# Performance work log

Hardware: AMD Instinct MI355X
Metric: run time of the kernel (lower is better)

Reference implementation:

```python
import jax, jax.numpy as jnp
import numpy as np

# ---- constants from __init__ ----
DT = 1.0
NX, NY = 192, 192
SRC_X, SRC_Y = 40, 96
PX = jnp.array([160, 160, 160])
PY = jnp.array([48, 96, 144])
PML_N, PML_P, PML_MAX = 20, 4.0, 3.0
C0, C1 = 1.0, 0.9
H = DT * 2.01 / 1.0  # grid spacing


def make_b():
    """PML damping profile b(x,y), [NX, NY]."""
    v = (PML_MAX * np.linspace(0.0, 1.0, PML_N + 1) ** PML_P).astype(np.float32)
    bx = np.zeros((NX, NY), np.float32)
    bx[: PML_N + 1, :] = v[::-1, None]
    bx[NX - PML_N - 1 :, :] = v[:, None]
    by = np.zeros((NX, NY), np.float32)
    by[:, : PML_N + 1] = v[::-1][None, :]
    by[:, NY - PML_N - 1 :] = v[None, :]
    return jnp.asarray(np.sqrt(bx ** 2 + by ** 2))


def _conv3(img, kern):
    # img [B,1,H,W], kern [1,1,3,3], 'same' padding
    return jax.lax.conv_general_dilated(
        img, kern, (1, 1), ((1, 1), (1, 1)),
        dimension_numbers=("NCHW", "OIHW", "NCHW"))


def _proj(x, eta=0.5, beta=100.0):
    return (jnp.tanh(beta * eta) + jnp.tanh(beta * (x - eta))) / (
        jnp.tanh(beta * eta) + jnp.tanh(beta * (1.0 - eta)))


def setup_inputs() -> dict:
    key = jax.random.key(0)
    k1, k2 = jax.random.split(key)
    x = jax.random.normal(k1, (4, 256), dtype=jnp.float32)  # [batch, T]
    rho = jax.random.uniform(k2, (NX, NY), dtype=jnp.float32)
    # clip_pml_rho(): rho[b != 0] = 0 for binarized model (applied at init)
    rho = jnp.where(make_b() != 0, 0.0, rho)
    return {"x": x, "rho": rho}


def reference(x, rho):
    b = make_b()
    lpf_k = jnp.array([[[[0.0, 0.125, 0.0], [0.125, 0.5, 0.125], [0.0, 0.125, 0.0]]]], jnp.float32)
    lap_k = (H ** -2) * jnp.array([[[[0.0, 1.0, 0.0], [1.0, -4.0, 1.0], [0.0, 1.0, 0.0]]]], jnp.float32)
    A1 = 1.0 / (DT ** -2 + b * 0.5 / DT)
    A2 = 2.0 * DT ** -2
    A3 = DT ** -2 - b * 0.5 / DT

    # binarized wave-speed field c(rho): LPF then tanh projection
    lpf_rho = _conv3(rho[None, None], lpf_k)[0, 0]
    c = C0 + (C1 - C0) * _proj(lpf_rho)
    c2 = c * c

    B = x.shape[0]
    y0 = jnp.zeros((B, NX, NY), x.dtype)

    def step(carry, xi):
        y1, y2 = carry
        lap = _conv3(y1[:, None], lap_k)[:, 0]            # [B,NX,NY]
        y = A1 * (A2 * y1 - A3 * y2 + c2 * lap)
        y = y.at[:, SRC_X, SRC_Y].add(xi)                 # source injection
        return (y, y1), y[:, PX, PY]                      # emit probe values [B,P]

    _, probes = jax.lax.scan(step, (y0, y0), x.T)         # probes [T,B,P]

    # integrate_probe_points: sum |y|^2 over time, normalize per batch
    I = jnp.sum(probes ** 2, axis=0)                      # [B,P]
    return I / jnp.sum(I, axis=1, keepdims=True)
```

## Files before the change

### kernel.cpp

```cpp
#include <hip/hip_runtime.h>
#include <math.h>

#define NXY    192
#define CELLS  (NXY*NXY)
#define NBATCH 4
#define NSTEPS 256
#define TCH    16
#define NCHUNK (NSTEPS/TCH)
#define TPB    512
#define NW     8
#define RPL    5
#define OUTR   6
#define NBLKS  256

#define K3_OFF (16*CELLS)
#define Q_OFF  (K3_OFF + CELLS)
#define I_OFF  (Q_OFF + CELLS)

typedef float v2f __attribute__((ext_vector_type(2)));

__device__ __forceinline__ float dpp_up1(float v) {
    int r = __builtin_amdgcn_update_dpp(0, __builtin_bit_cast(int, v),
                                        0x138, 0xf, 0xf, true);
    return __builtin_bit_cast(float, r);
}
__device__ __forceinline__ float dpp_dn1(float v) {
    int r = __builtin_amdgcn_update_dpp(0, __builtin_bit_cast(int, v),
                                        0x130, 0xf, 0xf, true);
    return __builtin_bit_cast(float, r);
}

__device__ __forceinline__ float pml_prof(int i) {
    int t;
    if (i <= 20)            t = 20 - i;
    else if (i >= NXY - 21) t = i - (NXY - 21);
    else                    return 0.0f;
    float u  = (float)t * 0.05f;
    float u2 = u * u;
    return 3.0f * u2 * u2;
}

__global__ void setup_k(const float* __restrict__ rho, float* __restrict__ ws) {
    int idx    = blockIdx.x * blockDim.x + threadIdx.x;
    int stride = gridDim.x * blockDim.x;
    for (int k = idx; k < 8 * CELLS; k += stride) ws[k] = 0.0f;
    const float IH2 = (float)(1.0 / (2.01 * 2.01));
    for (int k = idx; k < CELLS; k += stride) {
        int i = k / NXY, j = k % NXY;
        float r0 = rho[k];
        float ru = (i > 0)       ? rho[k - NXY] : 0.0f;
        float rd = (i < NXY - 1) ? rho[k + NXY] : 0.0f;
        float rl = (j > 0)       ? rho[k - 1]   : 0.0f;
        float rr2 = (j < NXY - 1) ? rho[k + 1]  : 0.0f;
        float lpf = 0.5f * r0 + 0.125f * ((ru + rd) + (rl + rr2));
        float p   = 0.5f * (1.0f + tanhf(100.0f * (lpf - 0.5f)));
        float c   = 1.0f - 0.1f * p;
        float c2h = c * c * IH2;
        float bx = pml_prof(i), by = pml_prof(j);
        float bb = sqrtf(bx * bx + by * by);
        float a1 = 1.0f / (1.0f + 0.5f * bb);
        ws[K3_OFF + k] = a1 * c2h;
        ws[Q_OFF  + k] = 1.0f - 2.0f * a1;
    }
    if (idx < 12) ws[I_OFF + idx] = 0.0f;
}

__global__ __launch_bounds__(TPB, 1)
void chunk_k(const float* __restrict__ x, float* __restrict__ ws, int chunk) {
    int blk = blockIdx.x;
    int b  = blk / 64;
    int r_ = blk % 64;
    int bi = r_ >> 1, cj = r_ & 1;
    int I0 = OUTR * bi - 17;
    int J0 = 96 * cj - 16;
    int t  = threadIdx.x;
    int w  = t >> 6;
    int l  = t & 63;
    int row0 = I0 + RPL * w;
    int gj   = J0 + 2 * l;

    __shared__ v2f hb[2][2][NW + 2][64];
    for (int k = t; k < 2 * 2 * (NW + 2) * 64; k += TPB)
        ((v2f*)hb)[k] = (v2f){0.f, 0.f};

    float xv[TCH];
    int xbase = b * NSTEPS + chunk * TCH;
#pragma unroll
    for (int i = 0; i < TCH; i++) xv[i] = x[xbase + i];

    const float* kg = ws + K3_OFF;
    const float* qg = ws + Q_OFF;
    int pin = chunk & 1, pout = pin ^ 1;
    const float* curg  = ws + ((pin  * 2 + 0) * NBATCH + b) * CELLS;
    const float* prvg  = ws + ((pin  * 2 + 1) * NBATCH + b) * CELLS;
    float*       ncurg = ws + ((pout * 2 + 0) * NBATCH + b) * CELLS;
    float*       nprvg = ws + ((pout * 2 + 1) * NBATCH + b) * CELLS;

    v2f yc[RPL], yp[RPL], Qa[RPL], Ka[RPL];
    bool cok = (gj >= 0 && gj < NXY);
#pragma unroll
    for (int r = 0; r < RPL; r++) {
        int gi = row0 + r;
        bool ok = cok && gi >= 0 && gi < NXY;
        v2f kv = {0.f,0.f}, qv = {0.f,0.f}, cv = {0.f,0.f}, pv = {0.f,0.f};
        if (ok) {
            int idx = gi * NXY + gj;
            kv = *(const v2f*)(kg + idx);
            qv = *(const v2f*)(qg + idx);
            cv = *(const v2f*)(curg + idx);
            pv = *(const v2f*)(prvg + idx);
        }
        yc[r] = cv; yp[r] = pv; Ka[r] = kv; Qa[r] = qv;
    }

    int sr = 40 - I0, sc = 96 - J0;
    bool wave_src = (sr >= RPL * w) && (sr < RPL * w + RPL);
    int src_rl = sr - RPL * w;
    float srcm = (2 * l == sc) ? 1.f : 0.f;

    int pcl = 2 * l + J0;
    bool wave_prb = (bi == 26) && (w == 4);
    const int prb_rl = 1;
    bool is_prb = (cj == 0) ? (pcl == 48) : (pcl == 96 || pcl == 144);
    float prbm = is_prb ? 1.f : 0.f;
    float pacc = 0.f;

    v2f uph, dnh;

#define ROWC(CUR, PRV, rr_, UP, DN, XSV, YN) do {                              \
    v2f cv = CUR[rr_];                                                         \
    float lf0 = dpp_up1(cv.y);                                                 \
    float rt1 = dpp_dn1(cv.x);                                                 \
    v2f h = (v2f){lf0, rt1} + __builtin_shufflevector(cv, cv, 1, 0);           \
    v2f S = ((UP) + (DN)) + h;                                                 \
    YN = cv + Qa[rr_] * (PRV[rr_] - cv) + Ka[rr_] * (S - 4.0f * cv);           \
    if (wave_src && (rr_) == src_rl) YN.x += srcm * (XSV);                     \
    if (wave_prb && (rr_) == prb_rl) { float q = prbm * YN.x; pacc += q * YN.x; } \
} while (0)

#define STEP(CUR, PRV, PH, SIDX) do {                                          \
    v2f t0, t4;                                                                \
    ROWC(CUR, PRV, 0, uph,    CUR[1], xv[SIDX], t0);                           \
    ROWC(CUR, PRV, 4, CUR[3], dnh,    xv[SIDX], t4);                           \
    hb[PH][0][w + 1][l] = t0;                                                  \
    hb[PH][1][w + 1][l] = t4;                                                  \
    PRV[0] = t0; PRV[4] = t4;                                                  \
    _Pragma("unroll")                                                          \
    for (int r = 1; r <= 3; r++) {                                             \
        v2f y;                                                                 \
        ROWC(CUR, PRV, r, CUR[r - 1], CUR[r + 1], xv[SIDX], y);                \
        PRV[r] = y;                                                            \
    }                                                                          \
    __syncthreads();                                                           \
    uph = hb[PH][1][w][l];                                                     \
    dnh = hb[PH][0][w + 2][l];                                                 \
} while (0)

    hb[0][0][w + 1][l] = yc[0];
    hb[0][1][w + 1][l] = yc[4];
    __syncthreads();
    uph = hb[0][1][w][l];
    dnh = hb[0][0][w + 2][l];

#pragma unroll
    for (int s2 = 0; s2 < TCH / 2; s2++) {
        STEP(yc, yp, 1, 2 * s2);
        STEP(yp, yc, 0, 2 * s2 + 1);
    }
#undef STEP
#undef ROWC

#pragma unroll
    for (int r = 0; r < RPL; r++) {
        int gi = row0 + r;
        if (gi >= OUTR * bi && gi < OUTR * bi + OUTR && l >= 8 && l < 56) {
            int idx = gi * NXY + gj;
            *(v2f*)(ncurg + idx) = yc[r];
            *(v2f*)(nprvg + idx) = yp[r];
        }
    }
    if (wave_prb && is_prb)
        ws[I_OFF + b * 3 + (pcl / 48 - 1)] += pacc;
}

__global__ void final_k(const float* __restrict__ ws, float* __restrict__ out) {
    int t = threadIdx.x;
    if (t < 12) {
        const float* I = ws + I_OFF;
        int b = t / 3;
        float s = I[3 * b] + I[3 * b + 1] + I[3 * b + 2];
        out[t] = I[t] / s;
    }
}

extern "C" void kernel_launch(void* const* d_in, const int* in_sizes, int n_in,
                              void* d_out, int out_size, void* d_ws, size_t ws_size,
                              hipStream_t stream) {
    const float* x   = (const float*)d_in[0];
    const float* rho = (const float*)d_in[1];
    float* ws  = (float*)d_ws;
    float* out = (float*)d_out;

    setup_k<<<256, 256, 0, stream>>>(rho, ws);
    for (int c = 0; c < NCHUNK; c++)
        chunk_k<<<NBLKS, TPB, 0, stream>>>(x, ws, c);
    final_k<<<1, 64, 0, stream>>>(ws, out);
}
```

Before: 203.0 us.

## Fuse setup, chunked steps and finalize into one persistent cooperative kernel

Replaces the setup kernel, the 16 per-chunk launches and the final kernel with a single cooperative launch that loops over chunks, using grid.sync between chunks. Each block now computes its own K/Q coefficients from rho in registers, which drops the global coefficient arrays and the workspace zeroing. It also keeps x in shared memory and remaps block indices across XCDs. The intent is to remove per-launch overhead and redundant global traffic, in exchange for grid-wide barrier cost and a requirement that all 256 blocks be co-resident.

```diff
diff --git a/kernel.cpp b/kernel.cpp
--- a/kernel.cpp
+++ b/kernel.cpp
@@ -1,5 +1,8 @@
 #include <hip/hip_runtime.h>
+#include <hip/hip_cooperative_groups.h>
 #include <math.h>
+
+namespace cg = cooperative_groups;
 
 #define NXY    192
 #define CELLS  (NXY*NXY)
@@ -13,9 +16,7 @@
 #define OUTR   6
 #define NBLKS  256
 
-#define K3_OFF (16*CELLS)
-#define Q_OFF  (K3_OFF + CELLS)
-#define I_OFF  (Q_OFF + CELLS)
+#define I_OFF  (16*CELLS)
 
 typedef float v2f __attribute__((ext_vector_type(2)));
 
@@ -40,34 +41,12 @@
     return 3.0f * u2 * u2;
 }
 
-__global__ void setup_k(const float* __restrict__ rho, float* __restrict__ ws) {
-    int idx    = blockIdx.x * blockDim.x + threadIdx.x;
-    int stride = gridDim.x * blockDim.x;
-    for (int k = idx; k < 8 * CELLS; k += stride) ws[k] = 0.0f;
-    const float IH2 = (float)(1.0 / (2.01 * 2.01));
-    for (int k = idx; k < CELLS; k += stride) {
-        int i = k / NXY, j = k % NXY;
-        float r0 = rho[k];
-        float ru = (i > 0)       ? rho[k - NXY] : 0.0f;
-        float rd = (i < NXY - 1) ? rho[k + NXY] : 0.0f;
-        float rl = (j > 0)       ? rho[k - 1]   : 0.0f;
-        float rr2 = (j < NXY - 1) ? rho[k + 1]  : 0.0f;
-        float lpf = 0.5f * r0 + 0.125f * ((ru + rd) + (rl + rr2));
-        float p   = 0.5f * (1.0f + tanhf(100.0f * (lpf - 0.5f)));
-        float c   = 1.0f - 0.1f * p;
-        float c2h = c * c * IH2;
-        float bx = pml_prof(i), by = pml_prof(j);
-        float bb = sqrtf(bx * bx + by * by);
-        float a1 = 1.0f / (1.0f + 0.5f * bb);
-        ws[K3_OFF + k] = a1 * c2h;
-        ws[Q_OFF  + k] = 1.0f - 2.0f * a1;
-    }
-    if (idx < 12) ws[I_OFF + idx] = 0.0f;
-}
-
 __global__ __launch_bounds__(TPB, 1)
-void chunk_k(const float* __restrict__ x, float* __restrict__ ws, int chunk) {
-    int blk = blockIdx.x;
+void wave_k(const float* __restrict__ x, const float* __restrict__ rho,
+            float* __restrict__ ws, float* __restrict__ out) {
+    cg::grid_group grid = cg::this_grid();
+
+    int blk = ((blockIdx.x & 7) << 5) | (blockIdx.x >> 3);
     int b  = blk / 64;
     int r_ = blk % 64;
     int bi = r_ >> 1, cj = r_ & 1;
@@ -80,38 +59,60 @@
     int gj   = J0 + 2 * l;
 
     __shared__ v2f hb[2][2][NW + 2][64];
+    __shared__ float xs[NSTEPS];
     for (int k = t; k < 2 * 2 * (NW + 2) * 64; k += TPB)
         ((v2f*)hb)[k] = (v2f){0.f, 0.f};
-
-    float xv[TCH];
-    int xbase = b * NSTEPS + chunk * TCH;
-#pragma unroll
-    for (int i = 0; i < TCH; i++) xv[i] = x[xbase + i];
-
-    const float* kg = ws + K3_OFF;
-    const float* qg = ws + Q_OFF;
-    int pin = chunk & 1, pout = pin ^ 1;
-    const float* curg  = ws + ((pin  * 2 + 0) * NBATCH + b) * CELLS;
-    const float* prvg  = ws + ((pin  * 2 + 1) * NBATCH + b) * CELLS;
-    float*       ncurg = ws + ((pout * 2 + 0) * NBATCH + b) * CELLS;
-    float*       nprvg = ws + ((pout * 2 + 1) * NBATCH + b) * CELLS;
-
-    v2f yc[RPL], yp[RPL], Qa[RPL], Ka[RPL];
+    if (t < NSTEPS) xs[t] = x[b * NSTEPS + t];
+
     bool cok = (gj >= 0 && gj < NXY);
-#pragma unroll
-    for (int r = 0; r < RPL; r++) {
-        int gi = row0 + r;
-        bool ok = cok && gi >= 0 && gi < NXY;
-        v2f kv = {0.f,0.f}, qv = {0.f,0.f}, cv = {0.f,0.f}, pv = {0.f,0.f};
-        if (ok) {
-            int idx = gi * NXY + gj;
-            kv = *(const v2f*)(kg + idx);
-            qv = *(const v2f*)(qg + idx);
-            cv = *(const v2f*)(curg + idx);
-            pv = *(const v2f*)(prvg + idx);
-        }
-        yc[r] = cv; yp[r] = pv; Ka[r] = kv; Qa[r] = qv;
+
+    v2f Ka[RPL], Qa[RPL];
+    {
+        v2f rv[RPL + 2];
+#pragma unroll
+        for (int r = 0; r < RPL + 2; r++) {
+            int gi = row0 - 1 + r;
+            bool ok = cok && gi >= 0 && gi < NXY;
+            rv[r] = ok ? *(const v2f*)(rho + gi * NXY + gj) : (v2f){0.f, 0.f};
+        }
+        const float IH2 = (float)(1.0 / (2.01 * 2.01));
+#pragma unroll
+        for (int r = 0; r < RPL; r++) {
+            int gi = row0 + r;
+            v2f rc = rv[r + 1], ru = rv[r], rd = rv[r + 2];
+            float lf = dpp_up1(rc.y);
+            float rt = dpp_dn1(rc.x);
+            float bx = pml_prof(gi);
+            v2f K, Q;
+            {
+                float lpf = 0.5f * rc.x + 0.125f * ((ru.x + rd.x) + (lf + rc.y));
+                float p   = 0.5f * (1.0f + tanhf(100.0f * (lpf - 0.5f)));
+                float c   = 1.0f - 0.1f * p;
+                float by  = pml_prof(gj);
+                float bb  = sqrtf(bx * bx + by * by);
+                float a1  = 1.0f / (1.0f + 0.5f * bb);
+                K.x = a1 * (c * c * IH2);
+                Q.x = 1.0f - 2.0f * a1;
+            }
+            {
+                float lpf = 0.5f * rc.y + 0.125f * ((ru.y + rd.y) + (rc.x + rt));
+                float p   = 0.5f * (1.0f + tanhf(100.0f * (lpf - 0.5f)));
+                float c   = 1.0f - 0.1f * p;
+                float by  = pml_prof(gj + 1);
+                float bb  = sqrtf(bx * bx + by * by);
+                float a1  = 1.0f / (1.0f + 0.5f * bb);
+                K.y = a1 * (c * c * IH2);
+                Q.y = 1.0f - 2.0f * a1;
+            }
+            bool ok = cok && gi >= 0 && gi < NXY;
+            Ka[r] = ok ? K : (v2f){0.f, 0.f};
+            Qa[r] = ok ? Q : (v2f){0.f, 0.f};
+        }
     }
+
+    v2f yc[RPL], yp[RPL];
+#pragma unroll
+    for (int r = 0; r < RPL; r++) { yc[r] = (v2f){0.f, 0.f}; yp[r] = (v2f){0.f, 0.f}; }
 
     int sr = 40 - I0, sc = 96 - J0;
     bool wave_src = (sr >= RPL * w) && (sr < RPL * w + RPL);
@@ -126,6 +127,7 @@
     float pacc = 0.f;
 
     v2f uph, dnh;
+    __syncthreads();
 
 #define ROWC(CUR, PRV, rr_, UP, DN, XSV, YN) do {                              \
     v2f cv = CUR[rr_];                                                         \
@@ -156,42 +158,72 @@
     dnh = hb[PH][0][w + 2][l];                                                 \
 } while (0)
 
-    hb[0][0][w + 1][l] = yc[0];
-    hb[0][1][w + 1][l] = yc[4];
-    __syncthreads();
-    uph = hb[0][1][w][l];
-    dnh = hb[0][0][w + 2][l];
-
-#pragma unroll
-    for (int s2 = 0; s2 < TCH / 2; s2++) {
-        STEP(yc, yp, 1, 2 * s2);
-        STEP(yp, yc, 0, 2 * s2 + 1);
+#pragma unroll 1
+    for (int chunk = 0; chunk < NCHUNK; chunk++) {
+        float xv[TCH];
+#pragma unroll
+        for (int i = 0; i < TCH; i++) xv[i] = xs[chunk * TCH + i];
+
+        if (chunk) {
+            int pin = chunk & 1;
+            const float* curg = ws + ((pin * 2 + 0) * NBATCH + b) * CELLS;
+            const float* prvg = ws + ((pin * 2 + 1) * NBATCH + b) * CELLS;
+#pragma unroll
+            for (int r = 0; r < RPL; r++) {
+                int gi = row0 + r;
+                bool ok = cok && gi >= 0 && gi < NXY;
+                v2f cv = {0.f, 0.f}, pv = {0.f, 0.f};
+                if (ok) {
+                    int idx = gi * NXY + gj;
+                    cv = *(const v2f*)(curg + idx);
+                    pv = *(const v2f*)(prvg + idx);
+                }
+                yc[r] = cv; yp[r] = pv;
+            }
+        }
+
+        hb[0][0][w + 1][l] = yc[0];
+        hb[0][1][w + 1][l] = yc[4];
+        __syncthreads();
+        uph = hb[0][1][w][l];
+        dnh = hb[0][0][w + 2][l];
+
+#pragma unroll
+        for (int s2 = 0; s2 < TCH / 2; s2++) {
+            STEP(yc, yp, 1, 2 * s2);
+            STEP(yp, yc, 0, 2 * s2 + 1);
+        }
+
+        if (chunk != NCHUNK - 1) {
+            int pout = (chunk & 1) ^ 1;
+            float* ncurg = ws + ((pout * 2 + 0) * NBATCH + b) * CELLS;
+            float* nprvg = ws + ((pout * 2 + 1) * NBATCH + b) * CELLS;
+#pragma unroll
+            for (int r = 0; r < RPL; r++) {
+                int gi = row0 + r;
+                if (gi >= OUTR * bi && gi < OUTR * bi + OUTR && l >= 8 && l < 56) {
+                    int idx = gi * NXY + gj;
+                    *(v2f*)(ncurg + idx) = yc[r];
+                    *(v2f*)(nprvg + idx) = yp[r];
+                }
+            }
+        } else {
+            if (wave_prb && is_prb)
+                ws[I_OFF + b * 3 + (pcl / 48 - 1)] = pacc;
+        }
+
+        grid.sync();
     }
+
+    if (blockIdx.x == 0 && t < 12) {
+        const float* I = ws + I_OFF;
+        int bb = t / 3;
+        float s = I[3 * bb] + I[3 * bb + 1] + I[3 * bb + 2];
+        out[t] = I[t] / s;
+    }
+}
 #undef STEP
 #undef ROWC
-
-#pragma unroll
-    for (int r = 0; r < RPL; r++) {
-        int gi = row0 + r;
-        if (gi >= OUTR * bi && gi < OUTR * bi + OUTR && l >= 8 && l < 56) {
-            int idx = gi * NXY + gj;
-            *(v2f*)(ncurg + idx) = yc[r];
-            *(v2f*)(nprvg + idx) = yp[r];
-        }
-    }
-    if (wave_prb && is_prb)
-        ws[I_OFF + b * 3 + (pcl / 48 - 1)] += pacc;
-}
-
-__global__ void final_k(const float* __restrict__ ws, float* __restrict__ out) {
-    int t = threadIdx.x;
-    if (t < 12) {
-        const float* I = ws + I_OFF;
-        int b = t / 3;
-        float s = I[3 * b] + I[3 * b + 1] + I[3 * b + 2];
-        out[t] = I[t] / s;
-    }
-}
 
 extern "C" void kernel_launch(void* const* d_in, const int* in_sizes, int n_in,
                               void* d_out, int out_size, void* d_ws, size_t ws_size,
@@ -199,10 +231,8 @@
     const float* x   = (const float*)d_in[0];
     const float* rho = (const float*)d_in[1];
     float* ws  = (float*)d_ws;
-    float* out = (float*)d_out;
-
-    setup_k<<<256, 256, 0, stream>>>(rho, ws);
-    for (int c = 0; c < NCHUNK; c++)
-        chunk_k<<<NBLKS, TPB, 0, stream>>>(x, ws, c);
-    final_k<<<1, 64, 0, stream>>>(ws, out);
-}
+    float* outp = (float*)d_out;
+
+    void* args[] = {(void*)&x, (void*)&rho, (void*)&ws, (void*)&outp};
+    hipLaunchCooperativeKernel(wave_k, dim3(NBLKS), dim3(TPB), args, 0, stream);
+}
```

Measured after the change: 607.9 us. 200% more time.
